# Performance work log

Measured on AMD Instinct MI355X. Metric: run time of the kernel, lower is better.

Reference implementation:

```python
import jax, jax.numpy as jnp
import numpy as np

EPS = 1e-5

def bn(x, g, b):
    # training-mode BatchNorm2d: normalize over all axes except channel axis 1
    ax = (0,) + tuple(range(2, x.ndim))
    m = x.mean(ax, keepdims=True)
    v = x.var(ax, keepdims=True)
    sh = (1, -1) + (1,) * (x.ndim - 2)
    return (x - m) * jax.lax.rsqrt(v + EPS) * g.reshape(sh) + b.reshape(sh)

def setup_inputs():
    key = jax.random.key(0)
    ks = jax.random.split(key, 7)
    N, C, H, W, G = 2, 128, 128, 128, 8
    gp = C // G  # group_planes = 16
    f32 = jnp.float32
    x = jax.random.normal(ks[0], (N, C, H, W), f32)
    wq = jax.random.normal(ks[1], (C // 2, C), f32) * np.float32(np.sqrt(1.0 / (C * gp)))
    wk = jax.random.normal(ks[2], (C // 2, C), f32) * np.float32(np.sqrt(1.0 / C))
    wv = jax.random.normal(ks[3], (C, C), f32) * np.float32(np.sqrt(1.0 / C))
    q_rel = jax.random.normal(ks[4], (gp // 2, 2 * H - 1), f32) * np.float32(np.sqrt(2.0 / C))
    k_rel = jax.random.normal(ks[5], (gp // 2, 2 * H - 1), f32) * np.float32(np.sqrt(2.0 / C))
    v_rel = jax.random.normal(ks[6], (gp, 2 * H - 1), f32) * np.float32(np.sqrt(1.0 / C))
    d = dict(x=x, wq=wq, wk=wk, wv=wv, q_rel=q_rel, k_rel=k_rel, v_rel=v_rel)
    for name, ch in [("bnq", C // 2), ("bnk", C // 2), ("bnv", C), ("bnqk", G), ("bnqr", G), ("bnkr", G), ("bnsv", C), ("bnsve", C)]:
        d[name + "_g"] = jnp.ones((ch,), f32)
        d[name + "_b"] = jnp.zeros((ch,), f32)
    return d

def reference(x, wq, wk, wv, q_rel, k_rel, v_rel, bnq_g, bnq_b, bnk_g, bnk_b, bnv_g, bnv_b, bnqk_g, bnqk_b, bnqr_g, bnqr_b, bnkr_g, bnkr_b, bnsv_g, bnsv_b, bnsve_g, bnsve_b):
    N, C, H, W = x.shape
    G = 8
    gp = C // G
    # 1x1 conv == channel matmul
    q = bn(jnp.einsum('oc,bchw->bohw', wq, x), bnq_g, bnq_b)
    k = bn(jnp.einsum('oc,bchw->bohw', wk, x), bnk_g, bnk_b)
    v = bn(jnp.einsum('oc,bchw->bohw', wv, x), bnv_g, bnv_b)
    # relative embedding gather: emb[c, j, i] = rel[c, j - i + H - 1]
    idx = jnp.arange(H)[:, None] - jnp.arange(H)[None, :] + (H - 1)  # [H, H]
    q_emb = q_rel[:, idx]
    k_emb = k_rel[:, idx]
    v_emb = v_rel[:, idx]
    qg = q.reshape(N, G, gp // 2, H, W)
    kg = k.reshape(N, G, gp // 2, H, W)
    vg = v.reshape(N, G, gp, H, W)
    qr = jnp.einsum('bgciw,cij->bgijw', qg, q_emb)
    qr = bn(qr.reshape(N, G, H * H, W), bnqr_g, bnqr_b).reshape(N, G, H, H, W)
    kr = jnp.einsum('bgciw,cij->bgijw', kg, k_emb)
    kr = bn(kr.reshape(N, G, H * H, W), bnkr_g, bnkr_b).reshape(N, G, H, H, W)
    kr = kr.transpose(0, 1, 3, 2, 4)
    qk = jnp.einsum('bgciw,bgcjw->bgijw', qg, kg)
    qk = bn(qk.reshape(N, G, H * H, W), bnqk_g, bnqk_b).reshape(N, G, H, H, W)
    sim = jax.nn.softmax(qk + qr + kr, axis=3)  # [N, G, H(i), H(j), W]
    sv = jnp.einsum('bgijw,bgcjw->bgciw', sim, vg).reshape(N, C, H, W)
    sve = jnp.einsum('bgijw,cji->bgciw', sim, v_emb).reshape(N, C, H, W)
    return bn(sv, bnsv_g, bnsv_b) + bn(sve, bnsve_g, bnsve_b)
```

## Files before the change

### kernel.cpp

```cpp
#include <hip/hip_runtime.h>
#include <hip/hip_fp16.h>


#define HW 16384

__device__ __forceinline__ float warp_sum(float v) {
#pragma unroll
  for (int o = 32; o > 0; o >>= 1) v += __shfl_down(v, o);
  return v;
}

__global__ __launch_bounds__(256) void k_transpose(const float* __restrict__ in, float* __restrict__ out) {
  __shared__ float t[32][33];
  int plane = blockIdx.y;
  int th = (blockIdx.x >> 2) * 32;
  int tw = (blockIdx.x & 3) * 32;
  const float* p = in + (size_t)plane * HW;
  float* q = out + (size_t)plane * HW;
  int lx = threadIdx.x, ly = threadIdx.y;
#pragma unroll
  for (int r = ly; r < 32; r += 8) t[r][lx] = p[(th + r) * 128 + tw + lx];
  __syncthreads();
#pragma unroll
  for (int r = ly; r < 32; r += 8) q[(tw + r) * 128 + th + lx] = t[lx][r];
}

__global__ __launch_bounds__(256) void k_wT(const float* __restrict__ wq, const float* __restrict__ wk,
                                            const float* __restrict__ wv, float* __restrict__ WT) {
  int idx = blockIdx.x * 256 + threadIdx.x;
  int och = idx & 255, c = idx >> 8;
  const float* wrow = och < 64 ? wq + och * 128 : (och < 128 ? wk + (och - 64) * 128 : wv + (och - 128) * 128);
  WT[c * 256 + och] = wrow[c];
}

__global__ __launch_bounds__(256) void k_qkv(const float* __restrict__ xT, const float* __restrict__ WT,
                                             float* __restrict__ qkvT) {
  __shared__ float Xs[64][64];
  __shared__ float Ws[64][64];
  int pb = blockIdx.x * 64;
  int ob = blockIdx.y * 64;
  int b = blockIdx.z;
  const float* xb = xT + (size_t)b * (128 * HW);
  int tid = threadIdx.x;
  int tx = tid & 15, ty = tid >> 4;
  float acc[4][4] = {};
  for (int ks = 0; ks < 2; ++ks) {
    for (int idx = tid; idx < 4096; idx += 256) {
      int c = idx >> 6, p = idx & 63;
      Xs[c][p] = xb[(ks * 64 + c) * HW + pb + p];
    }
    for (int idx = tid; idx < 4096; idx += 256) {
      int c = idx >> 6, o = idx & 63;
      Ws[c][o] = WT[(ks * 64 + c) * 256 + ob + o];
    }
    __syncthreads();
#pragma unroll 8
    for (int kk = 0; kk < 64; ++kk) {
      float a0 = Ws[kk][ty * 4 + 0], a1 = Ws[kk][ty * 4 + 1], a2 = Ws[kk][ty * 4 + 2], a3 = Ws[kk][ty * 4 + 3];
      float4 bv = *reinterpret_cast<const float4*>(&Xs[kk][tx * 4]);
      acc[0][0] += a0 * bv.x; acc[0][1] += a0 * bv.y; acc[0][2] += a0 * bv.z; acc[0][3] += a0 * bv.w;
      acc[1][0] += a1 * bv.x; acc[1][1] += a1 * bv.y; acc[1][2] += a1 * bv.z; acc[1][3] += a1 * bv.w;
      acc[2][0] += a2 * bv.x; acc[2][1] += a2 * bv.y; acc[2][2] += a2 * bv.z; acc[2][3] += a2 * bv.w;
      acc[3][0] += a3 * bv.x; acc[3][1] += a3 * bv.y; acc[3][2] += a3 * bv.z; acc[3][3] += a3 * bv.w;
    }
    __syncthreads();
  }
#pragma unroll
  for (int r = 0; r < 4; ++r) {
    int row = ob + ty * 4 + r;
    float4 o4 = make_float4(acc[r][0], acc[r][1], acc[r][2], acc[r][3]);
    *reinterpret_cast<float4*>(&qkvT[(size_t)(b * 256 + row) * HW + pb + tx * 4]) = o4;
  }
}

__global__ __launch_bounds__(256) void k_qkv_stats(const float* __restrict__ qkvT, double* __restrict__ statsQKV) {
  __shared__ float r1[4], r2[4];
  int ch = blockIdx.x;
  float s = 0.f, s2 = 0.f;
  for (int b = 0; b < 2; ++b) {
    const float* p = qkvT + (size_t)(b * 256 + ch) * HW;
    for (int idx = threadIdx.x; idx < HW; idx += 256) { float v = p[idx]; s += v; s2 += v * v; }
  }
  s = warp_sum(s); s2 = warp_sum(s2);
  int wid = threadIdx.x >> 6;
  if ((threadIdx.x & 63) == 0) { r1[wid] = s; r2[wid] = s2; }
  __syncthreads();
  if (threadIdx.x == 0) {
    statsQKV[2 * ch]     = (double)(r1[0] + r1[1] + r1[2] + r1[3]);
    statsQKV[2 * ch + 1] = (double)(r2[0] + r2[1] + r2[2] + r2[3]);
  }
}

__global__ __launch_bounds__(128) void k_rel_tables(const float* __restrict__ q_rel, const float* __restrict__ k_rel,
                                                    float* __restrict__ tabs) {
  int tbl = blockIdx.x / 44, item = blockIdx.x % 44;
  const float* rel = tbl ? k_rel : q_rel;
  float* out = tabs + tbl * 5632;
  int i = threadIdx.x;
  float s = 0.f;
  if (item < 8) {
    const float* r = rel + item * 255 + i;
    for (int d = 0; d < 128; ++d) s += r[d];
  } else {
    int p = item - 8;
    int pp = p, c = 0;
    while (pp >= 8 - c) { pp -= 8 - c; ++c; }
    int c2 = c + pp;
    const float* ra = rel + c * 255 + i;
    const float* rb = rel + c2 * 255 + i;
    for (int d = 0; d < 128; ++d) s += ra[d] * rb[d];
  }
  out[item * 128 + i] = s;
}

__global__ __launch_bounds__(128) void k_qkr_stats(
    const float* __restrict__ qkvT, const double* __restrict__ statsQKV,
    const float* __restrict__ bnq_g, const float* __restrict__ bnq_b,
    const float* __restrict__ bnk_g, const float* __restrict__ bnk_b,
    const float* __restrict__ tabs, double* __restrict__ statsA) {
  __shared__ float red[92][2];
  int slice = blockIdx.x;
  int w = slice & 127, g = (slice >> 7) & 7, b = slice >> 10;
  int i = threadIdx.x;
  float qn[8], kn[8];
  const float* qbase = qkvT + (size_t)(b * 256 + g * 8) * HW + w * 128 + i;
  const float* kbase = qkvT + (size_t)(b * 256 + 64 + g * 8) * HW + w * 128 + i;
#pragma unroll
  for (int c = 0; c < 8; ++c) {
    {
      int och = g * 8 + c;
      double su = statsQKV[2 * och], sq = statsQKV[2 * och + 1];
      double mu = su * (1.0 / 32768.0);
      float var = (float)(sq * (1.0 / 32768.0) - mu * mu);
      float sc = bnq_g[och] * rsqrtf(var + 1e-5f);
      qn[c] = qbase[c * HW] * sc + (bnq_b[och] - (float)mu * sc);
    }
    {
      int gi = g * 8 + c, och = 64 + gi;
      double su = statsQKV[2 * och], sq = statsQKV[2 * och + 1];
      double mu = su * (1.0 / 32768.0);
      float var = (float)(sq * (1.0 / 32768.0) - mu * mu);
      float sc = bnk_g[gi] * rsqrtf(var + 1e-5f);
      kn[c] = kbase[c * HW] * sc + (bnk_b[gi] - (float)mu * sc);
    }
  }
  float vals[92];
  int n = 0;
#pragma unroll
  for (int c = 0; c < 8; ++c) vals[n++] = qn[c];
#pragma unroll
  for (int c = 0; c < 8; ++c) vals[n++] = kn[c];
#pragma unroll
  for (int c = 0; c < 8; ++c)
#pragma unroll
    for (int c2 = c; c2 < 8; ++c2) vals[n++] = qn[c] * qn[c2];
#pragma unroll
  for (int c = 0; c < 8; ++c)
#pragma unroll
    for (int c2 = c; c2 < 8; ++c2) vals[n++] = kn[c] * kn[c2];
  float sqr = 0.f, s2qr = 0.f, skr = 0.f, s2kr = 0.f;
#pragma unroll
  for (int c = 0; c < 8; ++c) {
    sqr += qn[c] * tabs[c * 128 + i];
    skr += kn[c] * tabs[5632 + c * 128 + i];
  }
  {
    int p = 0;
#pragma unroll
    for (int c = 0; c < 8; ++c)
#pragma unroll
      for (int c2 = c; c2 < 8; ++c2) {
        float f = (c == c2) ? 1.f : 2.f;
        s2qr += f * qn[c] * qn[c2] * tabs[1024 + p * 128 + i];
        s2kr += f * kn[c] * kn[c2] * tabs[5632 + 1024 + p * 128 + i];
        ++p;
      }
  }
  vals[88] = sqr; vals[89] = s2qr; vals[90] = skr; vals[91] = s2kr;
  int lane = i & 63, wid = i >> 6;
#pragma unroll
  for (int vv = 0; vv < 92; ++vv) {
    float r = warp_sum(vals[vv]);
    if (lane == 0) red[vv][wid] = r;
  }
  __syncthreads();
  if (i == 0) {
    float f[92];
#pragma unroll
    for (int vv = 0; vv < 92; ++vv) f[vv] = red[vv][0] + red[vv][1];
    float sS = 0.f, s2S = 0.f;
#pragma unroll
    for (int c = 0; c < 8; ++c) sS += f[c] * f[8 + c];
    {
      int p = 0;
#pragma unroll
      for (int c = 0; c < 8; ++c)
#pragma unroll
        for (int c2 = c; c2 < 8; ++c2) { float fm = (c == c2) ? 1.f : 2.f; s2S += fm * f[16 + p] * f[52 + p]; ++p; }
    }
    atomicAdd(&statsA[(0 * 8 + g) * 2 + 0], (double)sS);
    atomicAdd(&statsA[(0 * 8 + g) * 2 + 1], (double)s2S);
    atomicAdd(&statsA[(1 * 8 + g) * 2 + 0], (double)f[88]);
    atomicAdd(&statsA[(1 * 8 + g) * 2 + 1], (double)f[89]);
    atomicAdd(&statsA[(2 * 8 + g) * 2 + 0], (double)f[90]);
    atomicAdd(&statsA[(2 * 8 + g) * 2 + 1], (double)f[91]);
  }
}

__global__ __launch_bounds__(256) void k_relT(const float* __restrict__ q_rel, const float* __restrict__ k_rel,
                                              float* __restrict__ relT) {
  int idx = blockIdx.x * 256 + threadIdx.x;
  if (idx < 2040) {
    int d = idx >> 3, c = idx & 7;
    relT[idx] = q_rel[c * 255 + d];
  } else if (idx < 4080) {
    int j = idx - 2040;
    int d = j >> 3, c = j & 7;
    relT[2040 + j] = k_rel[c * 255 + d];
  }
}

__global__ __launch_bounds__(256) void k_attn(
    const float* __restrict__ qkvT,
    const double* __restrict__ statsQKV, const double* __restrict__ statsA,
    const float* __restrict__ relTq, const float* __restrict__ relTk, const float* __restrict__ v_rel,
    const float* __restrict__ bnq_g, const float* __restrict__ bnq_b,
    const float* __restrict__ bnk_g, const float* __restrict__ bnk_b,
    const float* __restrict__ bnv_g, const float* __restrict__ bnv_b,
    const float* __restrict__ bnqk_g, const float* __restrict__ bnqk_b,
    const float* __restrict__ bnqr_g, const float* __restrict__ bnqr_b,
    const float* __restrict__ bnkr_g, const float* __restrict__ bnkr_b,
    float* __restrict__ svT, float* __restrict__ sveT) {
  __shared__ float Ks[4][128][8];
  __shared__ float Vs[4][128][16];
  __shared__ __half Wh[2][255][8];
  __shared__ float nsc[32], nsh[32];
  int tid = threadIdx.x;
  int slice0 = blockIdx.x * 4;
  int w0 = slice0 & 127, g = (slice0 >> 7) & 7, b = slice0 >> 10;
  if (tid < 32) {
    int och, gi; const float* gm; const float* bt;
    if (tid < 8)       { gi = g * 8 + tid;        och = gi;       gm = bnq_g; bt = bnq_b; }
    else if (tid < 16) { gi = g * 8 + (tid - 8);  och = 64 + gi;  gm = bnk_g; bt = bnk_b; }
    else               { gi = g * 16 + (tid - 16); och = 128 + gi; gm = bnv_g; bt = bnv_b; }
    double su = statsQKV[2 * och], sq = statsQKV[2 * och + 1];
    double mu = su * (1.0 / 32768.0);
    float var = (float)(sq * (1.0 / 32768.0) - mu * mu);
    float sc = gm[gi] * rsqrtf(var + 1e-5f);
    nsc[tid] = sc;
    nsh[tid] = bt[gi] - (float)mu * sc;
  }
  __syncthreads();
  for (int idx = tid; idx < 4096; idx += 256) {
    int j = idx & 127, c = (idx >> 7) & 7, s = idx >> 10;
    Ks[s][j][c] = qkvT[(size_t)(b * 256 + 64 + g * 8 + c) * HW + (w0 + s) * 128 + j] * nsc[8 + c] + nsh[8 + c];
  }
  for (int idx = tid; idx < 8192; idx += 256) {
    int j = idx & 127, c = (idx >> 7) & 15, s = idx >> 11;
    Vs[s][j][c] = qkvT[(size_t)(b * 256 + 128 + g * 16 + c) * HW + (w0 + s) * 128 + j] * nsc[16 + c] + nsh[16 + c];
  }
  for (int idx = tid; idx < 4080; idx += 256) {
    int c8 = idx / 2040, r = idx - c8 * 2040, d = r >> 3, e = r & 7;
    Wh[c8][d][e] = __float2half(v_rel[(c8 * 8 + e) * 255 + d]);
  }
  float aS, aQR, aKR, offs;
  {
    const double inv = 1.0 / 4194304.0;
    double s0 = statsA[(0 * 8 + g) * 2], q0 = statsA[(0 * 8 + g) * 2 + 1];
    double s1 = statsA[(1 * 8 + g) * 2], q1 = statsA[(1 * 8 + g) * 2 + 1];
    double s2 = statsA[(2 * 8 + g) * 2], q2 = statsA[(2 * 8 + g) * 2 + 1];
    double m0 = s0 * inv, m1 = s1 * inv, m2 = s2 * inv;
    float v0 = (float)(q0 * inv - m0 * m0);
    float v1 = (float)(q1 * inv - m1 * m1);
    float v2 = (float)(q2 * inv - m2 * m2);
    aS  = bnqk_g[g] * rsqrtf(v0 + 1e-5f);
    aQR = bnqr_g[g] * rsqrtf(v1 + 1e-5f);
    aKR = bnkr_g[g] * rsqrtf(v2 + 1e-5f);
    offs = (bnqk_b[g] - (float)m0 * aS) + (bnqr_b[g] - (float)m1 * aQR) + (bnkr_b[g] - (float)m2 * aKR);
    offs -= 5.545177444479562f;
  }
  __syncthreads();

  int wv = tid >> 6, lane = tid & 63;
  int slice = slice0 + wv, w = w0 + wv;
  int i0 = lane, i1 = lane + 64;
  float q0r[8], q1r[8];
  {
    const float* qbase = qkvT + (size_t)(b * 256 + g * 8) * HW + w * 128;
#pragma unroll
    for (int c = 0; c < 8; ++c) {
      q0r[c] = qbase[c * HW + i0] * nsc[c] + nsh[c];
      q1r[c] = qbase[c * HW + i1] * nsc[c] + nsh[c];
    }
  }
  float l0 = 0.f, l1 = 0.f;
  float asv0[16] = {}, asv1[16] = {};
  __half2 ha0[8], ha1[8];
#pragma unroll
  for (int u = 0; u < 8; ++u) { ha0[u] = __float2half2_rn(0.f); ha1[u] = __float2half2_rn(0.f); }
  const float* Kp = &Ks[wv][0][0];
  const float* Vp = &Vs[wv][0][0];

#pragma unroll 2
  for (int j = 0; j < 128; ++j) {
    float4 ka = *reinterpret_cast<const float4*>(Kp + j * 8);
    float4 kb = *reinterpret_cast<const float4*>(Kp + j * 8 + 4);
    int dq = 127 + i0 - j;
    int d0 = 127 - i0 + j;
    const float4* qp0 = reinterpret_cast<const float4*>(relTq + dq * 8);
    const float4* qp1 = reinterpret_cast<const float4*>(relTq + (dq + 64) * 8);
    const float4* rp0 = reinterpret_cast<const float4*>(relTk + d0 * 8);
    const float4* rp1 = reinterpret_cast<const float4*>(relTk + (d0 - 64) * 8);
    float4 qa0 = qp0[0], qb0 = qp0[1], qa1 = qp1[0], qb1 = qp1[1];
    float4 ra0 = rp0[0], rb0 = rp0[1], ra1 = rp1[0], rb1 = rp1[1];
    float S0 = q0r[0]*ka.x + q0r[1]*ka.y + q0r[2]*ka.z + q0r[3]*ka.w
             + q0r[4]*kb.x + q0r[5]*kb.y + q0r[6]*kb.z + q0r[7]*kb.w;
    float S1 = q1r[0]*ka.x + q1r[1]*ka.y + q1r[2]*ka.z + q1r[3]*ka.w
             + q1r[4]*kb.x + q1r[5]*kb.y + q1r[6]*kb.z + q1r[7]*kb.w;
    float QR0 = q0r[0]*qa0.x + q0r[1]*qa0.y + q0r[2]*qa0.z + q0r[3]*qa0.w
              + q0r[4]*qb0.x + q0r[5]*qb0.y + q0r[6]*qb0.z + q0r[7]*qb0.w;
    float QR1 = q1r[0]*qa1.x + q1r[1]*qa1.y + q1r[2]*qa1.z + q1r[3]*qa1.w
              + q1r[4]*qb1.x + q1r[5]*qb1.y + q1r[6]*qb1.z + q1r[7]*qb1.w;
    float KR0 = ka.x*ra0.x + ka.y*ra0.y + ka.z*ra0.z + ka.w*ra0.w
              + kb.x*rb0.x + kb.y*rb0.y + kb.z*rb0.z + kb.w*rb0.w;
    float KR1 = ka.x*ra1.x + ka.y*ra1.y + ka.z*ra1.z + ka.w*ra1.w
              + kb.x*rb1.x + kb.y*rb1.y + kb.z*rb1.z + kb.w*rb1.w;
    float a0 = fmaf(S0, aS, fmaf(QR0, aQR, fmaf(KR0, aKR, offs)));
    float a1 = fmaf(S1, aS, fmaf(QR1, aQR, fmaf(KR1, aKR, offs)));
    float e0 = __expf(a0);
    float e1 = __expf(a1);
    l0 += e0; l1 += e1;
    float4 v0 = *reinterpret_cast<const float4*>(Vp + j * 16);
    float4 v1 = *reinterpret_cast<const float4*>(Vp + j * 16 + 4);
    float4 v2 = *reinterpret_cast<const float4*>(Vp + j * 16 + 8);
    float4 v3 = *reinterpret_cast<const float4*>(Vp + j * 16 + 12);
    asv0[0]  += e0*v0.x; asv0[1]  += e0*v0.y; asv0[2]  += e0*v0.z; asv0[3]  += e0*v0.w;
    asv0[4]  += e0*v1.x; asv0[5]  += e0*v1.y; asv0[6]  += e0*v1.z; asv0[7]  += e0*v1.w;
    asv0[8]  += e0*v2.x; asv0[9]  += e0*v2.y; asv0[10] += e0*v2.z; asv0[11] += e0*v2.w;
    asv0[12] += e0*v3.x; asv0[13] += e0*v3.y; asv0[14] += e0*v3.z; asv0[15] += e0*v3.w;
    asv1[0]  += e1*v0.x; asv1[1]  += e1*v0.y; asv1[2]  += e1*v0.z; asv1[3]  += e1*v0.w;
    asv1[4]  += e1*v1.x; asv1[5]  += e1*v1.y; asv1[6]  += e1*v1.z; asv1[7]  += e1*v1.w;
    asv1[8]  += e1*v2.x; asv1[9]  += e1*v2.y; asv1[10] += e1*v2.z; asv1[11] += e1*v2.w;
    asv1[12] += e1*v3.x; asv1[13] += e1*v3.y; asv1[14] += e1*v3.z; asv1[15] += e1*v3.w;
    float4 wa0 = *reinterpret_cast<const float4*>(&Wh[0][d0][0]);
    float4 wb0 = *reinterpret_cast<const float4*>(&Wh[1][d0][0]);
    float4 wa1 = *reinterpret_cast<const float4*>(&Wh[0][d0 - 64][0]);
    float4 wb1 = *reinterpret_cast<const float4*>(&Wh[1][d0 - 64][0]);
    __half2 eh0 = __float2half2_rn(e0), eh1 = __float2half2_rn(e1);
    {
      const __half2* pa = reinterpret_cast<const __half2*>(&wa0);
      const __half2* pb = reinterpret_cast<const __half2*>(&wb0);
      ha0[0] = __hfma2(eh0, pa[0], ha0[0]); ha0[1] = __hfma2(eh0, pa[1], ha0[1]);
      ha0[2] = __hfma2(eh0, pa[2], ha0[2]); ha0[3] = __hfma2(eh0, pa[3], ha0[3]);
      ha0[4] = __hfma2(eh0, pb[0], ha0[4]); ha0[5] = __hfma2(eh0, pb[1], ha0[5]);
      ha0[6] = __hfma2(eh0, pb[2], ha0[6]); ha0[7] = __hfma2(eh0, pb[3], ha0[7]);
    }
    {
      const __half2* pa = reinterpret_cast<const __half2*>(&wa1);
      const __half2* pb = reinterpret_cast<const __half2*>(&wb1);
      ha1[0] = __hfma2(eh1, pa[0], ha1[0]); ha1[1] = __hfma2(eh1, pa[1], ha1[1]);
      ha1[2] = __hfma2(eh1, pa[2], ha1[2]); ha1[3] = __hfma2(eh1, pa[3], ha1[3]);
      ha1[4] = __hfma2(eh1, pb[0], ha1[4]); ha1[5] = __hfma2(eh1, pb[1], ha1[5]);
      ha1[6] = __hfma2(eh1, pb[2], ha1[6]); ha1[7] = __hfma2(eh1, pb[3], ha1[7]);
    }
  }
  float li0 = 1.f / l0, li1 = 1.f / l1;
  float* osv0  = svT  + (size_t)slice * 2048 + i0;
  float* osve0 = sveT + (size_t)slice * 2048 + i0;
  float* osv1  = svT  + (size_t)slice * 2048 + i1;
  float* osve1 = sveT + (size_t)slice * 2048 + i1;
#pragma unroll
  for (int c = 0; c < 16; ++c) {
    float h0 = (c & 1) ? __high2float(ha0[c >> 1]) : __low2float(ha0[c >> 1]);
    float h1 = (c & 1) ? __high2float(ha1[c >> 1]) : __low2float(ha1[c >> 1]);
    osv0[c * 128]  = asv0[c] * li0;
    osve0[c * 128] = h0 * li0;
    osv1[c * 128]  = asv1[c] * li1;
    osve1[c * 128] = h1 * li1;
  }
}

__global__ __launch_bounds__(256) void k_sv_stats(const float* __restrict__ svT, const float* __restrict__ sveT,
                                                  double* __restrict__ statsSV) {
  __shared__ float r1[4], r2[4];
  int ch = blockIdx.x;
  const float* base = (ch < 128) ? svT : sveT;
  int c = ch & 127, g = c >> 4, cc = c & 15;
  float s = 0.f, s2 = 0.f;
  for (int idx = threadIdx.x; idx < 32768; idx += 256) {
    int bw = idx >> 7, ii = idx & 127;
    int bb = bw >> 7, wwi = bw & 127;
    float v = base[(size_t)(((bb * 8 + g) * 128) + wwi) * 2048 + cc * 128 + ii];
    s += v; s2 += v * v;
  }
  s = warp_sum(s); s2 = warp_sum(s2);
  int wid = threadIdx.x >> 6;
  if ((threadIdx.x & 63) == 0) { r1[wid] = s; r2[wid] = s2; }
  __syncthreads();
  if (threadIdx.x == 0) {
    statsSV[2 * ch]     = (double)(r1[0] + r1[1] + r1[2] + r1[3]);
    statsSV[2 * ch + 1] = (double)(r2[0] + r2[1] + r2[2] + r2[3]);
  }
}

__global__ __launch_bounds__(256) void k_final(const float* __restrict__ svT, const float* __restrict__ sveT,
                                               const double* __restrict__ statsSV,
                                               const float* __restrict__ bnsv_g, const float* __restrict__ bnsv_b,
                                               const float* __restrict__ bnsve_g, const float* __restrict__ bnsve_b,
                                               float* __restrict__ out) {
  __shared__ float t[32][33];
  int plane = blockIdx.y;
  int b = plane >> 7, c = plane & 127;
  int g = c >> 4, cc = c & 15;
  double s = statsSV[2 * c], s2 = statsSV[2 * c + 1];
  double mu1 = s * (1.0 / 32768.0);
  float var1 = (float)(s2 * (1.0 / 32768.0) - mu1 * mu1);
  float sc1 = bnsv_g[c] * rsqrtf(var1 + 1e-5f);
  float sh1 = bnsv_b[c] - (float)mu1 * sc1;
  double se = statsSV[2 * (128 + c)], se2 = statsSV[2 * (128 + c) + 1];
  double mu2 = se * (1.0 / 32768.0);
  float var2 = (float)(se2 * (1.0 / 32768.0) - mu2 * mu2);
  float sc2 = bnsve_g[c] * rsqrtf(var2 + 1e-5f);
  float sh2 = bnsve_b[c] - (float)mu2 * sc2;
  int tw = (blockIdx.x & 3) * 32, ti = (blockIdx.x >> 2) * 32;
  int lx = threadIdx.x, ly = threadIdx.y;
#pragma unroll
  for (int r = ly; r < 32; r += 8) {
    int wr = tw + r, ii = ti + lx;
    size_t off = (size_t)((b * 8 + g) * 128 + wr) * 2048 + cc * 128 + ii;
    t[r][lx] = svT[off] * sc1 + sh1 + sveT[off] * sc2 + sh2;
  }
  __syncthreads();
#pragma unroll
  for (int r = ly; r < 32; r += 8)
    out[(size_t)plane * HW + (ti + r) * 128 + tw + lx] = t[lx][r];
}

extern "C" void kernel_launch(void* const* d_in, const int* in_sizes, int n_in,
                              void* d_out, int out_size, void* d_ws, size_t ws_size,
                              hipStream_t stream) {
  const float* x      = (const float*)d_in[0];
  const float* wq     = (const float*)d_in[1];
  const float* wk     = (const float*)d_in[2];
  const float* wv     = (const float*)d_in[3];
  const float* q_rel  = (const float*)d_in[4];
  const float* k_rel  = (const float*)d_in[5];
  const float* v_rel  = (const float*)d_in[6];
  const float* bnq_g  = (const float*)d_in[7];
  const float* bnq_b  = (const float*)d_in[8];
  const float* bnk_g  = (const float*)d_in[9];
  const float* bnk_b  = (const float*)d_in[10];
  const float* bnv_g  = (const float*)d_in[11];
  const float* bnv_b  = (const float*)d_in[12];
  const float* bnqk_g = (const float*)d_in[13];
  const float* bnqk_b = (const float*)d_in[14];
  const float* bnqr_g = (const float*)d_in[15];
  const float* bnqr_b = (const float*)d_in[16];
  const float* bnkr_g = (const float*)d_in[17];
  const float* bnkr_b = (const float*)d_in[18];
  const float* bnsv_g = (const float*)d_in[19];
  const float* bnsv_b = (const float*)d_in[20];
  const float* bnsve_g = (const float*)d_in[21];
  const float* bnsve_b = (const float*)d_in[22];
  float* out = (float*)d_out;

  float* wsf  = (float*)d_ws;
  float* xT   = wsf;
  float* svT  = wsf;
  float* qkvT = wsf + 4194304;
  float* sveT = wsf + 12582912;
  float* tabs = wsf + 16777216;
  float* relTq = tabs;
  float* relTk = tabs + 2040;
  float* WT   = wsf + 16788480;
  double* statsQKV = (double*)(wsf + 16821248);
  double* statsA   = statsQKV + 512;
  double* statsSV  = statsA + 48;

  hipMemsetAsync(statsA, 0, 48 * sizeof(double), stream);
  k_transpose<<<dim3(16, 256), dim3(32, 8), 0, stream>>>(x, xT);
  k_wT<<<128, 256, 0, stream>>>(wq, wk, wv, WT);
  k_qkv<<<dim3(256, 4, 2), 256, 0, stream>>>(xT, WT, qkvT);
  k_qkv_stats<<<256, 256, 0, stream>>>(qkvT, statsQKV);
  k_rel_tables<<<88, 128, 0, stream>>>(q_rel, k_rel, tabs);
  k_qkr_stats<<<2048, 128, 0, stream>>>(qkvT, statsQKV, bnq_g, bnq_b, bnk_g, bnk_b, tabs, statsA);
  k_relT<<<16, 256, 0, stream>>>(q_rel, k_rel, relTq);
  k_attn<<<512, 256, 0, stream>>>(qkvT, statsQKV, statsA, relTq, relTk, v_rel,
                                  bnq_g, bnq_b, bnk_g, bnk_b, bnv_g, bnv_b,
                                  bnqk_g, bnqk_b, bnqr_g, bnqr_b, bnkr_g, bnkr_b,
                                  svT, sveT);
  k_sv_stats<<<256, 256, 0, stream>>>(svT, sveT, statsSV);
  k_final<<<dim3(16, 256), dim3(32, 8), 0, stream>>>(svT, sveT, statsSV,
                                                     bnsv_g, bnsv_b, bnsve_g, bnsve_b, out);
  (void)in_sizes; (void)n_in; (void)out_size; (void)ws_size;
}
```

Measured before the change: 414.2 us.

## Use half-precision K/V and sv accumulation in attention, widen qkv GEMM tile

The attention kernel now stores normalized K and V in shared memory as fp16 and accumulates the softmax-weighted V sum with packed half2 FMAs, with the softmax offset constant raised to keep fp16 accumulators in range. This halves LDS footprint and LDS traffic and doubles FMA throughput for the sv accumulation, with a launch-bounds hint for occupancy. Separately, the qkv GEMM tile grows to 128 output channels per block with vectorized weight loads, halving the grid. The cost is reduced precision from fp16 storage and accumulation, which risks overflow or accuracy loss.

```diff
diff --git a/kernel.cpp b/kernel.cpp
--- a/kernel.cpp
+++ b/kernel.cpp
@@ -36,38 +36,43 @@
 __global__ __launch_bounds__(256) void k_qkv(const float* __restrict__ xT, const float* __restrict__ WT,
                                              float* __restrict__ qkvT) {
   __shared__ float Xs[64][64];
-  __shared__ float Ws[64][64];
+  __shared__ float Ws[64][128];
   int pb = blockIdx.x * 64;
-  int ob = blockIdx.y * 64;
+  int ob = blockIdx.y * 128;
   int b = blockIdx.z;
   const float* xb = xT + (size_t)b * (128 * HW);
   int tid = threadIdx.x;
   int tx = tid & 15, ty = tid >> 4;
-  float acc[4][4] = {};
+  float acc[8][4] = {};
   for (int ks = 0; ks < 2; ++ks) {
     for (int idx = tid; idx < 4096; idx += 256) {
       int c = idx >> 6, p = idx & 63;
       Xs[c][p] = xb[(ks * 64 + c) * HW + pb + p];
     }
-    for (int idx = tid; idx < 4096; idx += 256) {
-      int c = idx >> 6, o = idx & 63;
+    for (int idx = tid; idx < 8192; idx += 256) {
+      int c = idx >> 7, o = idx & 127;
       Ws[c][o] = WT[(ks * 64 + c) * 256 + ob + o];
     }
     __syncthreads();
-#pragma unroll 8
+#pragma unroll 4
     for (int kk = 0; kk < 64; ++kk) {
-      float a0 = Ws[kk][ty * 4 + 0], a1 = Ws[kk][ty * 4 + 1], a2 = Ws[kk][ty * 4 + 2], a3 = Ws[kk][ty * 4 + 3];
+      float4 a0 = *reinterpret_cast<const float4*>(&Ws[kk][ty * 8]);
+      float4 a1 = *reinterpret_cast<const float4*>(&Ws[kk][ty * 8 + 4]);
       float4 bv = *reinterpret_cast<const float4*>(&Xs[kk][tx * 4]);
-      acc[0][0] += a0 * bv.x; acc[0][1] += a0 * bv.y; acc[0][2] += a0 * bv.z; acc[0][3] += a0 * bv.w;
-      acc[1][0] += a1 * bv.x; acc[1][1] += a1 * bv.y; acc[1][2] += a1 * bv.z; acc[1][3] += a1 * bv.w;
-      acc[2][0] += a2 * bv.x; acc[2][1] += a2 * bv.y; acc[2][2] += a2 * bv.z; acc[2][3] += a2 * bv.w;
-      acc[3][0] += a3 * bv.x; acc[3][1] += a3 * bv.y; acc[3][2] += a3 * bv.z; acc[3][3] += a3 * bv.w;
+      acc[0][0] += a0.x * bv.x; acc[0][1] += a0.x * bv.y; acc[0][2] += a0.x * bv.z; acc[0][3] += a0.x * bv.w;
+      acc[1][0] += a0.y * bv.x; acc[1][1] += a0.y * bv.y; acc[1][2] += a0.y * bv.z; acc[1][3] += a0.y * bv.w;
+      acc[2][0] += a0.z * bv.x; acc[2][1] += a0.z * bv.y; acc[2][2] += a0.z * bv.z; acc[2][3] += a0.z * bv.w;
+      acc[3][0] += a0.w * bv.x; acc[3][1] += a0.w * bv.y; acc[3][2] += a0.w * bv.z; acc[3][3] += a0.w * bv.w;
+      acc[4][0] += a1.x * bv.x; acc[4][1] += a1.x * bv.y; acc[4][2] += a1.x * bv.z; acc[4][3] += a1.x * bv.w;
+      acc[5][0] += a1.y * bv.x; acc[5][1] += a1.y * bv.y; acc[5][2] += a1.y * bv.z; acc[5][3] += a1.y * bv.w;
+      acc[6][0] += a1.z * bv.x; acc[6][1] += a1.z * bv.y; acc[6][2] += a1.z * bv.z; acc[6][3] += a1.z * bv.w;
+      acc[7][0] += a1.w * bv.x; acc[7][1] += a1.w * bv.y; acc[7][2] += a1.w * bv.z; acc[7][3] += a1.w * bv.w;
     }
     __syncthreads();
   }
 #pragma unroll
-  for (int r = 0; r < 4; ++r) {
-    int row = ob + ty * 4 + r;
+  for (int r = 0; r < 8; ++r) {
+    int row = ob + ty * 8 + r;
     float4 o4 = make_float4(acc[r][0], acc[r][1], acc[r][2], acc[r][3]);
     *reinterpret_cast<float4*>(&qkvT[(size_t)(b * 256 + row) * HW + pb + tx * 4]) = o4;
   }
@@ -220,7 +225,7 @@
   }
 }
 
-__global__ __launch_bounds__(256) void k_attn(
+__global__ __launch_bounds__(256, 4) void k_attn(
     const float* __restrict__ qkvT,
     const double* __restrict__ statsQKV, const double* __restrict__ statsA,
     const float* __restrict__ relTq, const float* __restrict__ relTk, const float* __restrict__ v_rel,
@@ -231,8 +236,8 @@
     const float* __restrict__ bnqr_g, const float* __restrict__ bnqr_b,
     const float* __restrict__ bnkr_g, const float* __restrict__ bnkr_b,
     float* __restrict__ svT, float* __restrict__ sveT) {
-  __shared__ float Ks[4][128][8];
-  __shared__ float Vs[4][128][16];
+  __shared__ __half Ks[4][128][8];
+  __shared__ __half Vs[4][128][16];
   __shared__ __half Wh[2][255][8];
   __shared__ float nsc[32], nsh[32];
   int tid = threadIdx.x;
@@ -253,11 +258,13 @@
   __syncthreads();
   for (int idx = tid; idx < 4096; idx += 256) {
     int j = idx & 127, c = (idx >> 7) & 7, s = idx >> 10;
-    Ks[s][j][c] = qkvT[(size_t)(b * 256 + 64 + g * 8 + c) * HW + (w0 + s) * 128 + j] * nsc[8 + c] + nsh[8 + c];
+    Ks[s][j][c] = __float2half(
+        qkvT[(size_t)(b * 256 + 64 + g * 8 + c) * HW + (w0 + s) * 128 + j] * nsc[8 + c] + nsh[8 + c]);
   }
   for (int idx = tid; idx < 8192; idx += 256) {
     int j = idx & 127, c = (idx >> 7) & 15, s = idx >> 11;
-    Vs[s][j][c] = qkvT[(size_t)(b * 256 + 128 + g * 16 + c) * HW + (w0 + s) * 128 + j] * nsc[16 + c] + nsh[16 + c];
+    Vs[s][j][c] = __float2half(
+        qkvT[(size_t)(b * 256 + 128 + g * 16 + c) * HW + (w0 + s) * 128 + j] * nsc[16 + c] + nsh[16 + c]);
   }
   for (int idx = tid; idx < 4080; idx += 256) {
     int c8 = idx / 2040, r = idx - c8 * 2040, d = r >> 3, e = r & 7;
@@ -277,7 +284,7 @@
     aQR = bnqr_g[g] * rsqrtf(v1 + 1e-5f);
     aKR = bnkr_g[g] * rsqrtf(v2 + 1e-5f);
     offs = (bnqk_b[g] - (float)m0 * aS) + (bnqr_b[g] - (float)m1 * aQR) + (bnkr_b[g] - (float)m2 * aKR);
-    offs -= 5.545177444479562f;
+    offs -= 6.931471805599453f;
   }
   __syncthreads();
 
@@ -294,17 +301,23 @@
     }
   }
   float l0 = 0.f, l1 = 0.f;
-  float asv0[16] = {}, asv1[16] = {};
-  __half2 ha0[8], ha1[8];
-#pragma unroll
-  for (int u = 0; u < 8; ++u) { ha0[u] = __float2half2_rn(0.f); ha1[u] = __float2half2_rn(0.f); }
-  const float* Kp = &Ks[wv][0][0];
-  const float* Vp = &Vs[wv][0][0];
+  __half2 av0[8], av1[8], ha0[8], ha1[8];
+#pragma unroll
+  for (int u = 0; u < 8; ++u) {
+    av0[u] = __float2half2_rn(0.f); av1[u] = __float2half2_rn(0.f);
+    ha0[u] = __float2half2_rn(0.f); ha1[u] = __float2half2_rn(0.f);
+  }
+  const __half* Kp = &Ks[wv][0][0];
+  const __half* Vp = &Vs[wv][0][0];
 
 #pragma unroll 2
   for (int j = 0; j < 128; ++j) {
-    float4 ka = *reinterpret_cast<const float4*>(Kp + j * 8);
-    float4 kb = *reinterpret_cast<const float4*>(Kp + j * 8 + 4);
+    float4 kraw = *reinterpret_cast<const float4*>(Kp + j * 8);
+    const __half2* kh = reinterpret_cast<const __half2*>(&kraw);
+    float2 k01 = __half22float2(kh[0]);
+    float2 k23 = __half22float2(kh[1]);
+    float2 k45 = __half22float2(kh[2]);
+    float2 k67 = __half22float2(kh[3]);
     int dq = 127 + i0 - j;
     int d0 = 127 - i0 + j;
     const float4* qp0 = reinterpret_cast<const float4*>(relTq + dq * 8);
@@ -313,40 +326,40 @@
     const float4* rp1 = reinterpret_cast<const float4*>(relTk + (d0 - 64) * 8);
     float4 qa0 = qp0[0], qb0 = qp0[1], qa1 = qp1[0], qb1 = qp1[1];
     float4 ra0 = rp0[0], rb0 = rp0[1], ra1 = rp1[0], rb1 = rp1[1];
-    float S0 = q0r[0]*ka.x + q0r[1]*ka.y + q0r[2]*ka.z + q0r[3]*ka.w
-             + q0r[4]*kb.x + q0r[5]*kb.y + q0r[6]*kb.z + q0r[7]*kb.w;
-    float S1 = q1r[0]*ka.x + q1r[1]*ka.y + q1r[2]*ka.z + q1r[3]*ka.w
-             + q1r[4]*kb.x + q1r[5]*kb.y + q1r[6]*kb.z + q1r[7]*kb.w;
+    float S0 = q0r[0]*k01.x + q0r[1]*k01.y + q0r[2]*k23.x + q0r[3]*k23.y
+             + q0r[4]*k45.x + q0r[5]*k45.y + q0r[6]*k67.x + q0r[7]*k67.y;
+    float S1 = q1r[0]*k01.x + q1r[1]*k01.y + q1r[2]*k23.x + q1r[3]*k23.y
+             + q1r[4]*k45.x + q1r[5]*k45.y + q1r[6]*k67.x + q1r[7]*k67.y;
     float QR0 = q0r[0]*qa0.x + q0r[1]*qa0.y + q0r[2]*qa0.z + q0r[3]*qa0.w
               + q0r[4]*qb0.x + q0r[5]*qb0.y + q0r[6]*qb0.z + q0r[7]*qb0.w;
     float QR1 = q1r[0]*qa1.x + q1r[1]*qa1.y + q1r[2]*qa1.z + q1r[3]*qa1.w
               + q1r[4]*qb1.x + q1r[5]*qb1.y + q1r[6]*qb1.z + q1r[7]*qb1.w;
-    float KR0 = ka.x*ra0.x + ka.y*ra0.y + ka.z*ra0.z + ka.w*ra0.w
-              + kb.x*rb0.x + kb.y*rb0.y + kb.z*rb0.z + kb.w*rb0.w;
-    float KR1 = ka.x*ra1.x + ka.y*ra1.y + ka.z*ra1.z + ka.w*ra1.w
-              + kb.x*rb1.x + kb.y*rb1.y + kb.z*rb1.z + kb.w*rb1.w;
+    float KR0 = k01.x*ra0.x + k01.y*ra0.y + k23.x*ra0.z + k23.y*ra0.w
+              + k45.x*rb0.x + k45.y*rb0.y + k67.x*rb0.z + k67.y*rb0.w;
+    float KR1 = k01.x*ra1.x + k01.y*ra1.y + k23.x*ra1.z + k23.y*ra1.w
+              + k45.x*rb1.x + k45.y*rb1.y + k67.x*rb1.z + k67.y*rb1.w;
     float a0 = fmaf(S0, aS, fmaf(QR0, aQR, fmaf(KR0, aKR, offs)));
     float a1 = fmaf(S1, aS, fmaf(QR1, aQR, fmaf(KR1, aKR, offs)));
     float e0 = __expf(a0);
     float e1 = __expf(a1);
     l0 += e0; l1 += e1;
-    float4 v0 = *reinterpret_cast<const float4*>(Vp + j * 16);
-    float4 v1 = *reinterpret_cast<const float4*>(Vp + j * 16 + 4);
-    float4 v2 = *reinterpret_cast<const float4*>(Vp + j * 16 + 8);
-    float4 v3 = *reinterpret_cast<const float4*>(Vp + j * 16 + 12);
-    asv0[0]  += e0*v0.x; asv0[1]  += e0*v0.y; asv0[2]  += e0*v0.z; asv0[3]  += e0*v0.w;
-    asv0[4]  += e0*v1.x; asv0[5]  += e0*v1.y; asv0[6]  += e0*v1.z; asv0[7]  += e0*v1.w;
-    asv0[8]  += e0*v2.x; asv0[9]  += e0*v2.y; asv0[10] += e0*v2.z; asv0[11] += e0*v2.w;
-    asv0[12] += e0*v3.x; asv0[13] += e0*v3.y; asv0[14] += e0*v3.z; asv0[15] += e0*v3.w;
-    asv1[0]  += e1*v0.x; asv1[1]  += e1*v0.y; asv1[2]  += e1*v0.z; asv1[3]  += e1*v0.w;
-    asv1[4]  += e1*v1.x; asv1[5]  += e1*v1.y; asv1[6]  += e1*v1.z; asv1[7]  += e1*v1.w;
-    asv1[8]  += e1*v2.x; asv1[9]  += e1*v2.y; asv1[10] += e1*v2.z; asv1[11] += e1*v2.w;
-    asv1[12] += e1*v3.x; asv1[13] += e1*v3.y; asv1[14] += e1*v3.z; asv1[15] += e1*v3.w;
+    __half2 eh0 = __float2half2_rn(e0), eh1 = __float2half2_rn(e1);
+    float4 vraw0 = *reinterpret_cast<const float4*>(Vp + j * 16);
+    float4 vraw1 = *reinterpret_cast<const float4*>(Vp + j * 16 + 8);
+    const __half2* vh0 = reinterpret_cast<const __half2*>(&vraw0);
+    const __half2* vh1 = reinterpret_cast<const __half2*>(&vraw1);
+    av0[0] = __hfma2(eh0, vh0[0], av0[0]); av0[1] = __hfma2(eh0, vh0[1], av0[1]);
+    av0[2] = __hfma2(eh0, vh0[2], av0[2]); av0[3] = __hfma2(eh0, vh0[3], av0[3]);
+    av0[4] = __hfma2(eh0, vh1[0], av0[4]); av0[5] = __hfma2(eh0, vh1[1], av0[5]);
+    av0[6] = __hfma2(eh0, vh1[2], av0[6]); av0[7] = __hfma2(eh0, vh1[3], av0[7]);
+    av1[0] = __hfma2(eh1, vh0[0], av1[0]); av1[1] = __hfma2(eh1, vh0[1], av1[1]);
+    av1[2] = __hfma2(eh1, vh0[2], av1[2]); av1[3] = __hfma2(eh1, vh0[3], av1[3]);
+    av1[4] = __hfma2(eh1, vh1[0], av1[4]); av1[5] = __hfma2(eh1, vh1[1], av1[5]);
+    av1[6] = __hfma2(eh1, vh1[2], av1[6]); av1[7] = __hfma2(eh1, vh1[3], av1[7]);
     float4 wa0 = *reinterpret_cast<const float4*>(&Wh[0][d0][0]);
     float4 wb0 = *reinterpret_cast<const float4*>(&Wh[1][d0][0]);
     float4 wa1 = *reinterpret_cast<const float4*>(&Wh[0][d0 - 64][0]);
     float4 wb1 = *reinterpret_cast<const float4*>(&Wh[1][d0 - 64][0]);
-    __half2 eh0 = __float2half2_rn(e0), eh1 = __float2half2_rn(e1);
     {
       const __half2* pa = reinterpret_cast<const __half2*>(&wa0);
       const __half2* pb = reinterpret_cast<const __half2*>(&wb0);
@@ -371,11 +384,13 @@
   float* osve1 = sveT + (size_t)slice * 2048 + i1;
 #pragma unroll
   for (int c = 0; c < 16; ++c) {
+    float a0f = (c & 1) ? __high2float(av0[c >> 1]) : __low2float(av0[c >> 1]);
+    float a1f = (c & 1) ? __high2float(av1[c >> 1]) : __low2float(av1[c >> 1]);
     float h0 = (c & 1) ? __high2float(ha0[c >> 1]) : __low2float(ha0[c >> 1]);
     float h1 = (c & 1) ? __high2float(ha1[c >> 1]) : __low2float(ha1[c >> 1]);
-    osv0[c * 128]  = asv0[c] * li0;
+    osv0[c * 128]  = a0f * li0;
     osve0[c * 128] = h0 * li0;
-    osv1[c * 128]  = asv1[c] * li1;
+    osv1[c * 128]  = a1f * li1;
     osve1[c * 128] = h1 * li1;
   }
 }
@@ -480,7 +495,7 @@
   hipMemsetAsync(statsA, 0, 48 * sizeof(double), stream);
   k_transpose<<<dim3(16, 256), dim3(32, 8), 0, stream>>>(x, xT);
   k_wT<<<128, 256, 0, stream>>>(wq, wk, wv, WT);
-  k_qkv<<<dim3(256, 4, 2), 256, 0, stream>>>(xT, WT, qkvT);
+  k_qkv<<<dim3(256, 2, 2), 256, 0, stream>>>(xT, WT, qkvT);
   k_qkv_stats<<<256, 256, 0, stream>>>(qkvT, statsQKV);
   k_rel_tables<<<88, 128, 0, stream>>>(q_rel, k_rel, tabs);
   k_qkr_stats<<<2048, 128, 0, stream>>>(qkvT, statsQKV, bnq_g, bnq_b, bnk_g, bnk_b, tabs, statsA);
```

Result: slower. 447.7 us (+8.1%).
